# Optimization experiments

Measured on AMD Instinct MI355X. Metric: run time of the kernel, lower is better.

Reference implementation:

```python
import jax, jax.numpy as jnp
import numpy as np

EPS = 1e-6  # F.pairwise_distance default eps, added to the difference


def setup_inputs() -> dict:
    key = jax.random.key(0)
    k1, k2 = jax.random.split(key)
    N, NS, NQ, D = 2048, 5, 8, 256
    x = jax.random.normal(k1, (N, NS + NQ, D), dtype=jnp.float32)
    label = jax.random.randint(k2, (N,), 0, N, dtype=jnp.int64)
    return {"x": x, "label": label, "n_s": NS, "n_q": NQ}


def reference(x, label, n_s, n_q):
    # x: [N, n_s+n_q, D]
    anchors = jnp.mean(x[:, :n_s, :], axis=1)               # [N, D] prototypes
    N, D = anchors.shape
    queries = x[:, n_s:n_s + n_q, :].reshape(N * n_q, D)     # [N*n_q, D]

    # Exact ||q - a + eps||^2 via GEMM expansion (matches F.pairwise_distance(.,.)**2):
    # ||q-a||^2 + 2*eps*sum(q-a) + D*eps^2
    q_sq = jnp.sum(queries * queries, axis=-1)               # [N*n_q]
    a_sq = jnp.sum(anchors * anchors, axis=-1)               # [N]
    cross = queries @ anchors.T                              # [N*n_q, N]
    q_sum = jnp.sum(queries, axis=-1)                        # [N*n_q]
    a_sum = jnp.sum(anchors, axis=-1)                        # [N]
    dist_sq = (q_sq[:, None] + a_sq[None, :] - 2.0 * cross
               + 2.0 * EPS * (q_sum[:, None] - a_sum[None, :])
               + D * EPS * EPS)
    logits = -dist_sq                                        # [N*n_q, N]

    lab = jnp.repeat(label, n_q)                             # [N*n_q]
    logp = jax.nn.log_softmax(logits, axis=-1)
    nloss = -jnp.mean(jnp.take_along_axis(logp, lab[:, None], axis=1))
    prec1 = jnp.mean((jnp.argmax(logits, axis=-1) == lab).astype(jnp.float32)) * 100.0
    return nloss, prec1
```

## Files before the change

kernel.cpp:

```cpp
#include <hip/hip_runtime.h>
#include <math.h>

#define EPS  1e-6f
#define DD   256
#define NSUP 5
#define NQ   8
#define SEQ  13
#define L2E  1.44269504088896f
#define LN2  0.693147180559945f
#define NEP  2048
#define NROW 16384
#define NCOL 2048

typedef short bf16x8 __attribute__((ext_vector_type(8)));
typedef unsigned short u16x4 __attribute__((ext_vector_type(4)));
typedef float f32x4  __attribute__((ext_vector_type(4)));

__device__ __forceinline__ ushort f2bf(float f) {
  union { float f; unsigned u; } v; v.f = f;
  unsigned r = v.u + 0x7FFFu + ((v.u >> 16) & 1u);
  return (ushort)(r >> 16);
}
__device__ __forceinline__ float bf2f(short u) {
  union { unsigned u; float f; } v; v.u = ((unsigned)(unsigned short)u) << 16;
  return v.f;
}

__global__ __launch_bounds__(256) void proto_prep(
    const float* __restrict__ x, float* __restrict__ cb,
    ushort* __restrict__ Asw, ushort* __restrict__ Qsw,
    float* __restrict__ accum, int* __restrict__ fincount) {
  const int tid = threadIdx.x, g = tid >> 6, l = tid & 63;
  const int n = blockIdx.x * 4 + g;
  if (blockIdx.x == 0 && tid == 0) { accum[0] = 0.f; accum[1] = 0.f; fincount[0] = 0; }

  const float4* xr4 = (const float4*)(x + (size_t)n * SEQ * DD);

  const int d0   = l * 4;
  const int kk   = d0 >> 5, quad = (d0 >> 3) & 3, j = d0 & 7;
  const size_t chunk_d = (size_t)kk * 64 + (size_t)quad * 16;

  float4 a = {0.f, 0.f, 0.f, 0.f};
  #pragma unroll
  for (int s = 0; s < NSUP; ++s) {
    float4 v = xr4[s * 64 + l];
    a.x += v.x; a.y += v.y; a.z += v.z; a.w += v.w;
  }
  a.x *= 0.2f; a.y *= 0.2f; a.z *= 0.2f; a.w *= 0.2f;
  {
    const size_t idx = (((size_t)(n >> 4) * 8) * 64 + chunk_d + (n & 15)) * 8 + j;
    u16x4 o = {f2bf(a.x), f2bf(a.y), f2bf(a.z), f2bf(a.w)};
    *(u16x4*)(Asw + idx) = o;
  }
  float s1 = a.x + a.y + a.z + a.w;
  float s2 = a.x * a.x + a.y * a.y + a.z * a.z + a.w * a.w;
  #pragma unroll
  for (int off = 32; off; off >>= 1) {
    s1 += __shfl_xor(s1, off);
    s2 += __shfl_xor(s2, off);
  }
  if (l == 0) cb[n] = -L2E * (s2 - 2.f * EPS * s1);

  #pragma unroll
  for (int s = 0; s < NQ; ++s) {
    float4 q = xr4[(NSUP + s) * 64 + l];
    const int row = n * NQ + s;
    const size_t idx = (((size_t)(row >> 4) * 8) * 64 + chunk_d + (row & 15)) * 8 + j;
    u16x4 o = {f2bf(q.x), f2bf(q.y), f2bf(q.z), f2bf(q.w)};
    *(u16x4*)(Qsw + idx) = o;
  }
}

__global__ __launch_bounds__(256, 2) void proto_main(
    const ushort* __restrict__ Qsw, const ushort* __restrict__ Asw,
    const float* __restrict__ cb, const int* __restrict__ label,
    float* __restrict__ accum, int* __restrict__ fincount,
    float* __restrict__ out) {
  const int tid  = threadIdx.x;
  const int wid  = tid >> 6, lane = tid & 63;
  const int quad = lane >> 4, lcol = lane & 15;
  const int r0   = blockIdx.x * 32;

  const bf16x8* qb = (const bf16x8*)Qsw;
  const bf16x8* bb = (const bf16x8*)Asw;

  bf16x8 af[2][8];
  #pragma unroll
  for (int set = 0; set < 2; ++set) {
    const size_t base = ((size_t)((r0 >> 4) + set) * 8) * 64 + lane;
    #pragma unroll
    for (int kk = 0; kk < 8; ++kk) af[set][kk] = qb[base + (size_t)kk * 64];
  }

  float m[2][4], s[2][4];
  int   bi[2][4];
  #pragma unroll
  for (int set = 0; set < 2; ++set)
    #pragma unroll
    for (int i = 0; i < 4; ++i) {
      m[set][i] = -1e30f; s[set][i] = 0.f; bi[set][i] = 0x7fffffff;
    }

  auto process = [&](int T, bf16x8* B) {
    f32x4 c0 = {0.f, 0.f, 0.f, 0.f}, c1 = {0.f, 0.f, 0.f, 0.f};
    #pragma unroll
    for (int kk = 0; kk < 8; ++kk) {
      c0 = __builtin_amdgcn_mfma_f32_16x16x32_bf16(af[0][kk], B[kk], c0, 0, 0, 0);
      c1 = __builtin_amdgcn_mfma_f32_16x16x32_bf16(af[1][kk], B[kk], c1, 0, 0, 0);
    }
    const int   colIdx = T * 16 + lcol;
    const float cbv    = cb[colIdx];
    #pragma unroll
    for (int set = 0; set < 2; ++set) {
      #pragma unroll
      for (int i = 0; i < 4; ++i) {
        float cv = (set == 0) ? c0[i] : c1[i];
        float v2 = fmaf(cv, 2.f * L2E, cbv);
        float dv = v2 - m[set][i];
        bool  gt = dv > 0.f;
        float e  = exp2f(-fabsf(dv));
        s[set][i]  = fmaf(s[set][i], gt ? e : 1.f, gt ? 1.f : e);
        m[set][i]  = fmaxf(m[set][i], v2);
        bi[set][i] = gt ? colIdx : bi[set][i];
      }
    }
  };

  const int T0 = wid * 32;
  bf16x8 buf0[8], buf1[8];
  #pragma unroll
  for (int kk = 0; kk < 8; ++kk)
    buf0[kk] = bb[((size_t)T0 * 8 + (size_t)kk) * 64 + lane];

  #pragma unroll 1
  for (int t = 0; t < 32; t += 2) {
    {
      const int Tn = T0 + t + 1;
      #pragma unroll
      for (int kk = 0; kk < 8; ++kk)
        buf1[kk] = bb[((size_t)Tn * 8 + (size_t)kk) * 64 + lane];
    }
    process(T0 + t, buf0);
    {
      const int Tm = (t + 2 < 32) ? T0 + t + 2 : T0 + t + 1;
      #pragma unroll
      for (int kk = 0; kk < 8; ++kk)
        buf0[kk] = bb[((size_t)Tm * 8 + (size_t)kk) * 64 + lane];
    }
    process(T0 + t + 1, buf1);
  }

  #pragma unroll
  for (int mask = 1; mask < 16; mask <<= 1) {
    #pragma unroll
    for (int set = 0; set < 2; ++set)
      #pragma unroll
      for (int i = 0; i < 4; ++i) {
        float om = __shfl_xor(m[set][i], mask);
        float os = __shfl_xor(s[set][i], mask);
        int   oi = __shfl_xor(bi[set][i], mask);
        float nm = fmaxf(m[set][i], om);
        s[set][i] = s[set][i] * exp2f(m[set][i] - nm) + os * exp2f(om - nm);
        bool better = (om > m[set][i]) || (om == m[set][i] && oi < bi[set][i]);
        bi[set][i] = better ? oi : bi[set][i];
        m[set][i]  = nm;
      }
  }

  __shared__ float sm[4][32], ssh[4][32], slab[32];
  __shared__ int   sbi[4][32];
  if (lcol == 0) {
    #pragma unroll
    for (int set = 0; set < 2; ++set)
      #pragma unroll
      for (int i = 0; i < 4; ++i) {
        int rl = set * 16 + quad * 4 + i;
        sm[wid][rl] = m[set][i]; ssh[wid][rl] = s[set][i]; sbi[wid][rl] = bi[set][i];
      }
  }

  {
    const int r = tid >> 3, l = tid & 7;
    const int row = r0 + r;
    const int lab = label[row >> 3];
    const size_t qbase = ((size_t)(row >> 4) * 8 + l) * 64 + (row & 15);
    const size_t abase = ((size_t)(lab >> 4) * 8 + l) * 64 + (lab & 15);
    float dot = 0.f;
    #pragma unroll
    for (int q16 = 0; q16 < 4; ++q16) {
      bf16x8 qv = qb[qbase + (size_t)q16 * 16];
      bf16x8 av = bb[abase + (size_t)q16 * 16];
      #pragma unroll
      for (int j = 0; j < 8; ++j) dot = fmaf(bf2f(qv[j]), bf2f(av[j]), dot);
    }
    #pragma unroll
    for (int mask = 1; mask < 8; mask <<= 1) dot += __shfl_xor(dot, mask);
    if (l == 0) slab[r] = fmaf(dot, 2.f * L2E, cb[lab]);
  }
  __syncthreads();

  if (tid < 32) {
    float mm = sm[0][tid], sv = ssh[0][tid];
    int   b  = sbi[0][tid];
    #pragma unroll
    for (int w = 1; w < 4; ++w) {
      float om = sm[w][tid], os = ssh[w][tid];
      int   oi = sbi[w][tid];
      float nm = fmaxf(mm, om);
      sv = sv * exp2f(mm - nm) + os * exp2f(om - nm);
      bool better = (om > mm) || (om == mm && oi < b);
      b = better ? oi : b;
      mm = nm;
    }
    const int row = r0 + tid;
    const int lb  = label[row >> 3];
    float loss = LN2 * (mm + log2f(sv) - slab[tid]);
    float corr = (b == lb) ? 1.f : 0.f;
    #pragma unroll
    for (int mask = 16; mask; mask >>= 1) {
      loss += __shfl_xor(loss, mask);
      corr += __shfl_xor(corr, mask);
    }
    if (tid == 0) {
      atomicAdd(&accum[0], loss);
      atomicAdd(&accum[1], corr);
      __threadfence();
      if (atomicAdd(fincount, 1) == (int)gridDim.x - 1) {
        out[0] = atomicAdd(&accum[0], 0.f) / (float)NROW;
        out[1] = atomicAdd(&accum[1], 0.f) * 100.f / (float)NROW;
      }
    }
  }
}

extern "C" void kernel_launch(void* const* d_in, const int* in_sizes, int n_in,
                              void* d_out, int out_size, void* d_ws, size_t ws_size,
                              hipStream_t stream) {
  const float* x     = (const float*)d_in[0];
  const int*   label = (const int*)d_in[1];
  float* out = (float*)d_out;

  float*  W        = (float*)d_ws;
  float*  accum    = W;
  int*    fincount = (int*)(W + 2);
  float*  cb       = W + 16;
  ushort* Asw      = (ushort*)(cb + NCOL);
  ushort* Qsw      = Asw + (size_t)NCOL * DD;

  hipLaunchKernelGGL(proto_prep, dim3(NEP / 4), dim3(256), 0, stream,
                     x, cb, Asw, Qsw, accum, fincount);
  hipLaunchKernelGGL(proto_main, dim3(NROW / 32), dim3(256), 0, stream,
                     Qsw, Asw, cb, label, accum, fincount, out);
}
```

Baseline: 123.1 us.

## Stream anchor tiles via direct global-to-LDS loads with double buffering

Each wave's anchor tiles are now brought into a per-wave double-buffered LDS region with global_load_lds instead of prefetching into register buffers, and read back from LDS before each MFMA. The column bias values for the wave are staged into shared memory once up front. The aim is to cut the registers spent on the two 8-fragment prefetch buffers, which could raise occupancy, and to overlap the global loads with compute. In exchange it adds about 80KB of LDS per block, which may cap occupancy below the launch bound of 2. It also relies on a hand-coded waitcnt immediate that must correctly wait for the previous tile's DMA while leaving the next one in flight.

```diff
diff --git a/kernel.cpp b/kernel.cpp
--- a/kernel.cpp
+++ b/kernel.cpp
@@ -81,8 +81,18 @@
   const int quad = lane >> 4, lcol = lane & 15;
   const int r0   = blockIdx.x * 32;
 
+  __shared__ __align__(16) ushort smem[4][2][4096];
+  __shared__ float scb[4][512];
+  __shared__ float sm[4][32], ssh[4][32], slab[32];
+  __shared__ int   sbi[4][32];
+
   const bf16x8* qb = (const bf16x8*)Qsw;
   const bf16x8* bb = (const bf16x8*)Asw;
+  const int T0 = wid * 32;
+
+  #pragma unroll
+  for (int i = 0; i < 8; ++i)
+    scb[wid][i * 64 + lane] = cb[T0 * 16 + i * 64 + lane];
 
   bf16x8 af[2][8];
   #pragma unroll
@@ -101,15 +111,35 @@
       m[set][i] = -1e30f; s[set][i] = 0.f; bi[set][i] = 0x7fffffff;
     }
 
-  auto process = [&](int T, bf16x8* B) {
+  auto dma_tile = [&](int T, int bufi) {
+    const ushort* src = Asw + ((size_t)T * 8) * 512 + (size_t)lane * 8;
+    #pragma unroll
+    for (int kk = 0; kk < 8; ++kk)
+      __builtin_amdgcn_global_load_lds(
+          (const __attribute__((address_space(1))) void*)(src + kk * 512),
+          (__attribute__((address_space(3))) void*)(&smem[wid][bufi][kk * 512]),
+          16, 0, 0);
+  };
+
+  dma_tile(T0, 0);
+
+  #pragma unroll 1
+  for (int t = 0; t < 32; ++t) {
+    const int Tn = (t + 1 < 32) ? T0 + t + 1 : T0 + t;
+    dma_tile(Tn, (t + 1) & 1);
+    __builtin_amdgcn_s_waitcnt(0xF78);
+    __builtin_amdgcn_sched_barrier(0);
+
+    const ushort* B = &smem[wid][t & 1][0];
     f32x4 c0 = {0.f, 0.f, 0.f, 0.f}, c1 = {0.f, 0.f, 0.f, 0.f};
     #pragma unroll
     for (int kk = 0; kk < 8; ++kk) {
-      c0 = __builtin_amdgcn_mfma_f32_16x16x32_bf16(af[0][kk], B[kk], c0, 0, 0, 0);
-      c1 = __builtin_amdgcn_mfma_f32_16x16x32_bf16(af[1][kk], B[kk], c1, 0, 0, 0);
-    }
-    const int   colIdx = T * 16 + lcol;
-    const float cbv    = cb[colIdx];
+      bf16x8 b = *(const bf16x8*)(B + kk * 512 + lane * 8);
+      c0 = __builtin_amdgcn_mfma_f32_16x16x32_bf16(af[0][kk], b, c0, 0, 0, 0);
+      c1 = __builtin_amdgcn_mfma_f32_16x16x32_bf16(af[1][kk], b, c1, 0, 0, 0);
+    }
+    const int   colIdx = (T0 + t) * 16 + lcol;
+    const float cbv    = scb[wid][t * 16 + lcol];
     #pragma unroll
     for (int set = 0; set < 2; ++set) {
       #pragma unroll
@@ -124,30 +154,6 @@
         bi[set][i] = gt ? colIdx : bi[set][i];
       }
     }
-  };
-
-  const int T0 = wid * 32;
-  bf16x8 buf0[8], buf1[8];
-  #pragma unroll
-  for (int kk = 0; kk < 8; ++kk)
-    buf0[kk] = bb[((size_t)T0 * 8 + (size_t)kk) * 64 + lane];
-
-  #pragma unroll 1
-  for (int t = 0; t < 32; t += 2) {
-    {
-      const int Tn = T0 + t + 1;
-      #pragma unroll
-      for (int kk = 0; kk < 8; ++kk)
-        buf1[kk] = bb[((size_t)Tn * 8 + (size_t)kk) * 64 + lane];
-    }
-    process(T0 + t, buf0);
-    {
-      const int Tm = (t + 2 < 32) ? T0 + t + 2 : T0 + t + 1;
-      #pragma unroll
-      for (int kk = 0; kk < 8; ++kk)
-        buf0[kk] = bb[((size_t)Tm * 8 + (size_t)kk) * 64 + lane];
-    }
-    process(T0 + t + 1, buf1);
   }
 
   #pragma unroll
@@ -167,8 +173,6 @@
       }
   }
 
-  __shared__ float sm[4][32], ssh[4][32], slab[32];
-  __shared__ int   sbi[4][32];
   if (lcol == 0) {
     #pragma unroll
     for (int set = 0; set < 2; ++set)
```

Result: slower. 130.9 us (+6.4%).
